# Performance work log

Measured on AMD Instinct MI355X. Metric: run time of the kernel, lower is better.

## Reference

```python
import jax, jax.numpy as jnp
import numpy as np

B, T, OBS, S, OUT, H = 128, 2048, 128, 128, 64, 64
SCALE = 0.05  # keep the linear recurrence numerically stable over T steps


def setup_inputs() -> dict:
    key = jax.random.key(0)
    ks = jax.random.split(key, 8)
    return {
        "obs": jax.random.normal(ks[0], (B, T, OBS), dtype=jnp.float32),
        "x0": jnp.zeros((B, S), dtype=jnp.float32),
        "A_T": SCALE * jax.random.normal(ks[1], (S, S), dtype=jnp.float32),
        "By_T": SCALE * jax.random.normal(ks[2], (OBS, S), dtype=jnp.float32),
        "Cu_T": SCALE * jax.random.normal(ks[3], (S, OUT), dtype=jnp.float32),
        "Duy_T": SCALE * jax.random.normal(ks[4], (OBS, OUT), dtype=jnp.float32),
        "log_stds": jnp.full((OUT,), -1.6094379124341003, dtype=jnp.float32),
        "W0": SCALE * jax.random.normal(ks[5], (H, OBS), dtype=jnp.float32),
        "b0": jnp.zeros((H,), dtype=jnp.float32),
        "W1": SCALE * jax.random.normal(ks[6], (H, H), dtype=jnp.float32),
        "b1": jnp.zeros((H,), dtype=jnp.float32),
        "W2": SCALE * jax.random.normal(ks[7], (1, H), dtype=jnp.float32),
        "b2": jnp.zeros((1,), dtype=jnp.float32),
        "dt": jnp.float32(0.01),
    }


def reference(obs, x0, A_T, By_T, Cu_T, Duy_T, log_stds, W0, b0, W1, b1, W2, b2, dt):
    def xdot(x, y):
        return x @ A_T + y @ By_T

    def step(x, y):
        # control output at current state, then RK4 integration of x' = A x + B y
        u = x @ Cu_T + y @ Duy_T                      # [B, OUT]
        k1 = xdot(x, y)
        k2 = xdot(x + dt * k1 / 2, y)
        k3 = xdot(x + dt * k2 / 2, y)
        k4 = xdot(x + dt * k3, y)
        x_next = x + dt / 6 * (k1 + 2 * k2 + 2 * k3 + k4)
        return x_next, u

    obs_t = jnp.swapaxes(obs, 0, 1)                   # [T, B, OBS]
    x_final, actions_t = jax.lax.scan(step, x0, obs_t)
    actions = jnp.swapaxes(actions_t, 0, 1)           # [B, T, OUT]

    logs = jnp.broadcast_to(log_stds, (actions.shape[0], actions.shape[1], log_stds.shape[0]))
    outputs = jnp.concatenate([actions, logs], axis=2)  # [B, T, 2*OUT]

    # value MLP: Linear -> tanh -> Linear -> tanh -> Linear
    h = jnp.tanh(obs @ W0.T + b0)
    h = jnp.tanh(h @ W1.T + b1)
    cur_value = (h @ W2.T + b2).reshape(-1)           # [B*T]

    return outputs, cur_value, x_final
```

## Files before the change

### kernel.cpp

```cpp
#include <hip/hip_runtime.h>
#include <hip/hip_bf16.h>

#define B_    128
#define T_    2048
#define OBS_  128
#define S_    128
#define OUT_  64
#define H_    64
#define NR    (B_*T_)
#define K_CH  32
#define C_CH  64
#define VOFF  (NR*2*OUT_)
#define XFOFF (VOFF + NR)

typedef __attribute__((ext_vector_type(8))) short short8v;
typedef __attribute__((ext_vector_type(4))) float f32x4;

__device__ __forceinline__ unsigned short f2bf_hw(float f){
  __hip_bfloat16 h = __float2bfloat16(f);
  union { __hip_bfloat16 hh; unsigned short u; } cv; cv.hh = h; return cv.u;
}
__device__ __forceinline__ unsigned int pk2(float a, float b){
  __hip_bfloat162 h = __float22bfloat162_rn(make_float2(a, b));
  union { __hip_bfloat162 h2; unsigned int u; } cv; cv.h2 = h; return cv.u;
}
__device__ __forceinline__ float bf2f(unsigned short h){
  return __uint_as_float(((unsigned int)h) << 16);
}
__device__ __forceinline__ float fast_tanh(float x){
  float z = __builtin_exp2f(x * 2.88539008f);
  return 1.f - 2.f * __builtin_amdgcn_rcpf(z + 1.f);
}

__global__ __launch_bounds__(256) void k_mm(const float* __restrict__ A,
                                            const float* __restrict__ B,
                                            float* __restrict__ C, int ldc){
  int e = blockIdx.x * 256 + threadIdx.x;
  int r = e >> 7, c = e & 127;
  float acc = 0.f;
  #pragma unroll 4
  for (int k = 0; k < 128; ++k) acc += A[r*128 + k] * B[k*128 + c];
  C[r*ldc + c] = acc;
}

__global__ __launch_bounds__(256) void k_mm2(const float* __restrict__ A_T,
                                             const float* __restrict__ A2,
                                             float* __restrict__ A3,
                                             float* __restrict__ A4){
  int e = blockIdx.x * 256 + threadIdx.x;
  int r = e >> 7, c = e & 127;
  float a3 = 0.f, a4 = 0.f;
  #pragma unroll 4
  for (int k = 0; k < 128; ++k){
    float l = A2[r*128 + k];
    a3 += l * A_T[k*128 + c];
    a4 += l * A2[k*128 + c];
  }
  A3[e] = a3; A4[e] = a4;
}

__global__ __launch_bounds__(256) void k_build(const float* __restrict__ A_T,
                                               const float* __restrict__ A2,
                                               const float* __restrict__ A3,
                                               const float* __restrict__ A4,
                                               const float* __restrict__ Cu_T,
                                               const float* __restrict__ Duy_T,
                                               const float* __restrict__ dtp,
                                               float* __restrict__ M,
                                               unsigned short* __restrict__ MmiT,
                                               float* __restrict__ P, float* __restrict__ Wcat,
                                               unsigned short* __restrict__ cubT){
  float dt = *dtp;
  float d2 = dt*dt*0.5f;
  float d3 = d2*dt*(1.f/3.f);
  float d4 = d3*dt*0.25f;
  int e = blockIdx.x * 256 + threadIdx.x;
  int r = e >> 7, c = e & 127;
  float eye = (r == c) ? 1.f : 0.f;
  float mi = dt*A_T[e] + d2*A2[e] + d3*A3[e] + d4*A4[e];
  M[e] = eye + mi;
  MmiT[c*128 + r] = f2bf_hw(mi);
  P[e] = dt*eye + d2*A_T[e] + d3*A2[e] + d4*A3[e];
  if (e < 128*64){
    int k = e >> 6, o = e & 63;
    Wcat[k*192 + 128 + o] = Duy_T[e];
    cubT[o*128 + k] = f2bf_hw(Cu_T[e]);
  }
}

__global__ __launch_bounds__(256) void k_gm2(const float* __restrict__ By_T,
                                             const float* __restrict__ Pp,
                                             const float* __restrict__ Mm,
                                             float* __restrict__ Wcat,
                                             float* __restrict__ sq1){
  int e = blockIdx.x * 256 + threadIdx.x;
  int r = e >> 7, c = e & 127;
  float ga = 0.f, m2 = 0.f;
  #pragma unroll 4
  for (int k = 0; k < 128; ++k){
    ga += By_T[r*128 + k] * Pp[k*128 + c];
    m2 += Mm[r*128 + k] * Mm[k*128 + c];
  }
  Wcat[r*192 + c] = ga;
  sq1[e] = m2;
}

__global__ __launch_bounds__(256) void k_m4cvt(const float* __restrict__ sq1,
                                               const float* __restrict__ Wcat,
                                               const float* __restrict__ W0,
                                               const float* __restrict__ W1,
                                               float* __restrict__ sq2,
                                               unsigned short* __restrict__ WbfT,
                                               unsigned short* __restrict__ W0bf,
                                               unsigned short* __restrict__ W1bf){
  int e = blockIdx.x * 256 + threadIdx.x;
  int r = e >> 7, c = e & 127;
  float m4 = 0.f;
  #pragma unroll 4
  for (int k = 0; k < 128; ++k) m4 += sq1[r*128 + k] * sq1[k*128 + c];
  sq2[e] = m4;
  for (int i = e; i < 24576; i += 16384)
    WbfT[(i % 192)*128 + (i / 192)] = f2bf_hw(Wcat[i]);
  if (e < 8192) W0bf[e] = f2bf_hw(W0[e]);
  if (e < 4096) W1bf[e] = f2bf_hw(W1[e]);
}

__global__ __launch_bounds__(256) void k_fused(const float* __restrict__ obs,
                                               const unsigned short* __restrict__ WbfT,
                                               const unsigned short* __restrict__ W0bf,
                                               const unsigned short* __restrict__ W1bf,
                                               const float* __restrict__ W2,
                                               const float* __restrict__ b0g,
                                               const float* __restrict__ b1g,
                                               const float* __restrict__ b2g,
                                               unsigned short* __restrict__ cuy,
                                               float* __restrict__ out){
  __shared__ __align__(16) unsigned short ylds[64*136];
  __shared__ __align__(16) unsigned short ct[2][16*200];
  __shared__ __align__(16) unsigned short h0l[64*80];
  __shared__ float pl[64][4];
  int tid = threadIdx.x;
  int lane = tid & 63, w = tid >> 6;
  size_t row0 = (size_t)blockIdx.x * 128;
  int colbase = w * 48;
  int colh    = w * 16;
  int lr = lane & 15;
  int lk = (lane >> 4) * 8;

  short8v bfrag[3][4];
  #pragma unroll
  for (int cf = 0; cf < 3; ++cf)
    #pragma unroll
    for (int kk = 0; kk < 4; ++kk)
      bfrag[cf][kk] = *(const short8v*)&WbfT[(size_t)(colbase + cf*16 + lr)*128 + kk*32 + lk];
  short8v bw0[4];
  #pragma unroll
  for (int kk = 0; kk < 4; ++kk)
    bw0[kk] = *(const short8v*)&W0bf[(size_t)(colh + lr)*128 + kk*32 + lk];
  short8v bw1[2];
  #pragma unroll
  for (int kk = 0; kk < 2; ++kk)
    bw1[kk] = *(const short8v*)&W1bf[(size_t)(colh + lr)*64 + kk*32 + lk];
  float b0v = b0g[colh + lr];
  float b1v = b1g[colh + lr];
  float w2v = W2[colh + lr];

  for (int h = 0; h < 2; ++h){
    {
      int base = tid * 32;
      int r = base >> 7, c0 = base & 127;
      const float* grow = obs + (row0 + h*64 + r) * 128;
      #pragma unroll
      for (int it = 0; it < 4; ++it){
        float4 a0 = *(const float4*)&grow[c0 + it*8];
        float4 a1 = *(const float4*)&grow[c0 + it*8 + 4];
        uint4 pv;
        pv.x = pk2(a0.x, a0.y); pv.y = pk2(a0.z, a0.w);
        pv.z = pk2(a1.x, a1.y); pv.w = pk2(a1.z, a1.w);
        *(uint4*)&ylds[r*136 + c0 + it*8] = pv;
      }
    }
    __syncthreads();
    for (int rfh = 0; rfh < 4; ++rfh){
      f32x4 acc0 = {0.f,0.f,0.f,0.f}, acc1 = {0.f,0.f,0.f,0.f}, acc2 = {0.f,0.f,0.f,0.f};
      f32x4 acch = {0.f,0.f,0.f,0.f};
      #pragma unroll
      for (int kk = 0; kk < 4; ++kk){
        short8v af = *(const short8v*)&ylds[(rfh*16 + lr)*136 + kk*32 + lk];
        acc0 = __builtin_amdgcn_mfma_f32_16x16x32_bf16(af, bfrag[0][kk], acc0, 0, 0, 0);
        acc1 = __builtin_amdgcn_mfma_f32_16x16x32_bf16(af, bfrag[1][kk], acc1, 0, 0, 0);
        acc2 = __builtin_amdgcn_mfma_f32_16x16x32_bf16(af, bfrag[2][kk], acc2, 0, 0, 0);
        acch = __builtin_amdgcn_mfma_f32_16x16x32_bf16(af, bw0[kk],     acch, 0, 0, 0);
      }
      int hrow = rfh*16 + (lane >> 4)*4;
      int crow = (lane >> 4)*4;
      unsigned short* ctb = ct[rfh & 1];
      #pragma unroll
      for (int j = 0; j < 4; ++j){
        ctb[(crow + j)*200 + colbase      + lr] = f2bf_hw(acc0[j]);
        ctb[(crow + j)*200 + colbase + 16 + lr] = f2bf_hw(acc1[j]);
        ctb[(crow + j)*200 + colbase + 32 + lr] = f2bf_hw(acc2[j]);
        h0l[(hrow + j)*80 + colh + lr]          = f2bf_hw(fast_tanh(acch[j] + b0v));
      }
      __syncthreads();
      for (int li = tid; li < 16*24; li += 256){
        int r = li / 24, seg = li % 24;
        *(uint4*)&cuy[(row0 + h*64 + rfh*16 + r)*192 + seg*8] = *(const uint4*)&ctb[r*200 + seg*8];
      }
    }
    for (int rf = 0; rf < 4; ++rf){
      f32x4 acc = {b1v, b1v, b1v, b1v};
      #pragma unroll
      for (int kk = 0; kk < 2; ++kk){
        short8v af = *(const short8v*)&h0l[(rf*16 + lr)*80 + kk*32 + lk];
        acc = __builtin_amdgcn_mfma_f32_16x16x32_bf16(af, bw1[kk], acc, 0, 0, 0);
      }
      float4 vpart;
      #pragma unroll
      for (int j = 0; j < 4; ++j) (&vpart.x)[j] = fast_tanh(acc[j]) * w2v;
      #pragma unroll
      for (int m = 1; m < 16; m <<= 1){
        vpart.x += __shfl_xor(vpart.x, m);
        vpart.y += __shfl_xor(vpart.y, m);
        vpart.z += __shfl_xor(vpart.z, m);
        vpart.w += __shfl_xor(vpart.w, m);
      }
      if (lr == 0){
        int hrow = rf*16 + (lane >> 4)*4;
        #pragma unroll
        for (int j = 0; j < 4; ++j) pl[hrow + j][w] = (&vpart.x)[j];
      }
    }
    __syncthreads();
    if (tid < 64)
      out[(size_t)VOFF + row0 + h*64 + tid] = pl[tid][0] + pl[tid][1] + pl[tid][2] + pl[tid][3] + b2g[0];
    __syncthreads();
  }
}

__global__ __launch_bounds__(256) void k_phase1(const unsigned short* __restrict__ cuy,
                                                const unsigned short* __restrict__ MmiT,
                                                float* __restrict__ Dd){
  __shared__ __align__(16) unsigned short xwA[16*136];
  __shared__ __align__(16) unsigned short xwB[16*136];
  int tid = threadIdx.x;
  int lane = tid & 63, w = tid >> 6;
  int lr = lane & 15, lg = lane >> 4;
  int pr = blockIdx.x >> 3, bi = blockIdx.x & 7;
  int b0 = bi*16;
  int ciA = 2*pr, ciB = 2*pr + 1;
  int t0A = ciA*K_CH, t0B = ciB*K_CH;
  int colbase = w*32;

  short8v bm[2][4];
  #pragma unroll
  for (int ctt = 0; ctt < 2; ++ctt)
    #pragma unroll
    for (int kk = 0; kk < 4; ++kk)
      bm[ctt][kk] = *(const short8v*)&MmiT[(size_t)(colbase + ctt*16 + lr)*128 + kk*32 + lg*8];

  f32x4 accA[2], accB[2];
  #pragma unroll
  for (int ctt = 0; ctt < 2; ++ctt)
    #pragma unroll
    for (int j = 0; j < 4; ++j){
      size_t rb = (size_t)(b0 + lg*4 + j)*T_;
      accA[ctt][j] = bf2f(cuy[(rb + t0A)*192 + colbase + ctt*16 + lr]);
      accB[ctt][j] = bf2f(cuy[(rb + t0B)*192 + colbase + ctt*16 + lr]);
    }

  for (int s = 1; s < K_CH; ++s){
    unsigned short cnA[2][4], cnB[2][4];
    #pragma unroll
    for (int ctt = 0; ctt < 2; ++ctt)
      #pragma unroll
      for (int j = 0; j < 4; ++j){
        size_t rb = (size_t)(b0 + lg*4 + j)*T_;
        cnA[ctt][j] = cuy[(rb + t0A + s)*192 + colbase + ctt*16 + lr];
        cnB[ctt][j] = cuy[(rb + t0B + s)*192 + colbase + ctt*16 + lr];
      }
    #pragma unroll
    for (int ctt = 0; ctt < 2; ++ctt)
      #pragma unroll
      for (int j = 0; j < 4; ++j){
        xwA[(lg*4 + j)*136 + colbase + ctt*16 + lr] = f2bf_hw(accA[ctt][j]);
        xwB[(lg*4 + j)*136 + colbase + ctt*16 + lr] = f2bf_hw(accB[ctt][j]);
      }
    __syncthreads();
    short8v afA[4], afB[4];
    #pragma unroll
    for (int kk = 0; kk < 4; ++kk){
      afA[kk] = *(const short8v*)&xwA[lr*136 + kk*32 + lg*8];
      afB[kk] = *(const short8v*)&xwB[lr*136 + kk*32 + lg*8];
    }
    __syncthreads();
    #pragma unroll
    for (int ctt = 0; ctt < 2; ++ctt)
      #pragma unroll
      for (int kk = 0; kk < 4; ++kk)
        accA[ctt] = __builtin_amdgcn_mfma_f32_16x16x32_bf16(afA[kk], bm[ctt][kk], accA[ctt], 0, 0, 0);
    #pragma unroll
    for (int ctt = 0; ctt < 2; ++ctt)
      #pragma unroll
      for (int kk = 0; kk < 4; ++kk)
        accB[ctt] = __builtin_amdgcn_mfma_f32_16x16x32_bf16(afB[kk], bm[ctt][kk], accB[ctt], 0, 0, 0);
    #pragma unroll
    for (int ctt = 0; ctt < 2; ++ctt)
      #pragma unroll
      for (int j = 0; j < 4; ++j){
        accA[ctt][j] += bf2f(cnA[ctt][j]);
        accB[ctt][j] += bf2f(cnB[ctt][j]);
      }
  }
  #pragma unroll
  for (int ctt = 0; ctt < 2; ++ctt)
    #pragma unroll
    for (int j = 0; j < 4; ++j){
      Dd[(size_t)ciA*16384 + (size_t)(b0 + lg*4 + j)*128 + colbase + ctt*16 + lr] = accA[ctt][j];
      Dd[(size_t)ciB*16384 + (size_t)(b0 + lg*4 + j)*128 + colbase + ctt*16 + lr] = accB[ctt][j];
    }
}

__global__ __launch_bounds__(256) void k_combine(const float* __restrict__ Mk,
                                                 const float* __restrict__ Dd,
                                                 const float* __restrict__ x0,
                                                 float* __restrict__ XS,
                                                 float* __restrict__ xfin){
  __shared__ float xl[128];
  __shared__ float pl[256];
  int tid = threadIdx.x;
  int b = blockIdx.x;
  int c = tid & 127, h = tid >> 7;
  float mreg[64];
  #pragma unroll
  for (int j = 0; j < 64; ++j) mreg[j] = Mk[(64*h + j)*128 + c];
  if (tid < 128) xl[tid] = x0[(size_t)b*128 + tid];
  float dcur = (tid < 128) ? Dd[(size_t)b*128 + tid] : 0.f;
  __syncthreads();
  for (int i = 0; i < C_CH; ++i){
    if (tid < 128) XS[(size_t)i*16384 + (size_t)b*128 + tid] = xl[tid];
    float dnext = 0.f;
    if (i + 1 < C_CH && tid < 128)
      dnext = Dd[(size_t)(i+1)*16384 + (size_t)b*128 + tid];
    float part = 0.f;
    #pragma unroll
    for (int jj = 0; jj < 64; jj += 4){
      float4 xv = *(const float4*)&xl[64*h + jj];
      part += xv.x*mreg[jj] + xv.y*mreg[jj+1] + xv.z*mreg[jj+2] + xv.w*mreg[jj+3];
    }
    pl[tid] = part;
    __syncthreads();
    if (tid < 128)
      xl[tid] = pl[tid] + pl[tid + 128] + dcur;
    __syncthreads();
    dcur = dnext;
  }
  if (tid < 128) xfin[(size_t)b*128 + tid] = xl[tid];
}

__global__ __launch_bounds__(256) void k_phase3(const unsigned short* __restrict__ cuy,
                                                const unsigned short* __restrict__ MmiT,
                                                const unsigned short* __restrict__ cubT,
                                                const float* __restrict__ XS,
                                                const float* __restrict__ ls,
                                                float* __restrict__ out){
  __shared__ __align__(16) unsigned short xwA[16*136];
  __shared__ __align__(16) unsigned short xwB[16*136];
  int tid = threadIdx.x;
  int lane = tid & 63, w = tid >> 6;
  int lr = lane & 15, lg = lane >> 4;
  int pr = blockIdx.x >> 3, bi = blockIdx.x & 7;
  int b0 = bi*16;
  int ciA = 2*pr, ciB = 2*pr + 1;
  int t0A = ciA*K_CH, t0B = ciB*K_CH;
  int colbase = w*32;
  int ucolbase = w*16;
  float lsv = ls[ucolbase + lr];

  short8v bm[2][4];
  #pragma unroll
  for (int ctt = 0; ctt < 2; ++ctt)
    #pragma unroll
    for (int kk = 0; kk < 4; ++kk)
      bm[ctt][kk] = *(const short8v*)&MmiT[(size_t)(colbase + ctt*16 + lr)*128 + kk*32 + lg*8];
  short8v bc[4];
  #pragma unroll
  for (int kk = 0; kk < 4; ++kk)
    bc[kk] = *(const short8v*)&cubT[(size_t)(ucolbase + lr)*128 + kk*32 + lg*8];

  f32x4 accA[2], accB[2];
  #pragma unroll
  for (int ctt = 0; ctt < 2; ++ctt)
    #pragma unroll
    for (int j = 0; j < 4; ++j){
      size_t xb = (size_t)(b0 + lg*4 + j)*128 + colbase + ctt*16 + lr;
      accA[ctt][j] = XS[(size_t)ciA*16384 + xb];
      accB[ctt][j] = XS[(size_t)ciB*16384 + xb];
    }

  for (int s = 0; s < K_CH; ++s){
    f32x4 auA, auB;
    #pragma unroll
    for (int j = 0; j < 4; ++j){
      size_t rb = (size_t)(b0 + lg*4 + j)*T_;
      auA[j] = bf2f(cuy[(rb + t0A + s)*192 + 128 + ucolbase + lr]);
      auB[j] = bf2f(cuy[(rb + t0B + s)*192 + 128 + ucolbase + lr]);
    }
    unsigned short cnA[2][4], cnB[2][4];
    if (s + 1 < K_CH){
      #pragma unroll
      for (int ctt = 0; ctt < 2; ++ctt)
        #pragma unroll
        for (int j = 0; j < 4; ++j){
          size_t rb = (size_t)(b0 + lg*4 + j)*T_;
          cnA[ctt][j] = cuy[(rb + t0A + s)*192 + colbase + ctt*16 + lr];
          cnB[ctt][j] = cuy[(rb + t0B + s)*192 + colbase + ctt*16 + lr];
        }
    }
    #pragma unroll
    for (int ctt = 0; ctt < 2; ++ctt)
      #pragma unroll
      for (int j = 0; j < 4; ++j){
        xwA[(lg*4 + j)*136 + colbase + ctt*16 + lr] = f2bf_hw(accA[ctt][j]);
        xwB[(lg*4 + j)*136 + colbase + ctt*16 + lr] = f2bf_hw(accB[ctt][j]);
      }
    __syncthreads();
    short8v afA[4], afB[4];
    #pragma unroll
    for (int kk = 0; kk < 4; ++kk){
      afA[kk] = *(const short8v*)&xwA[lr*136 + kk*32 + lg*8];
      afB[kk] = *(const short8v*)&xwB[lr*136 + kk*32 + lg*8];
    }
    __syncthreads();
    #pragma unroll
    for (int kk = 0; kk < 4; ++kk){
      auA = __builtin_amdgcn_mfma_f32_16x16x32_bf16(afA[kk], bc[kk], auA, 0, 0, 0);
      auB = __builtin_amdgcn_mfma_f32_16x16x32_bf16(afB[kk], bc[kk], auB, 0, 0, 0);
    }
    #pragma unroll
    for (int j = 0; j < 4; ++j){
      size_t rb = (size_t)(b0 + lg*4 + j)*T_;
      out[(rb + t0A + s)*128 + ucolbase + lr]       = auA[j];
      out[(rb + t0A + s)*128 + 64 + ucolbase + lr]  = lsv;
      out[(rb + t0B + s)*128 + ucolbase + lr]       = auB[j];
      out[(rb + t0B + s)*128 + 64 + ucolbase + lr]  = lsv;
    }
    if (s + 1 < K_CH){
      #pragma unroll
      for (int ctt = 0; ctt < 2; ++ctt)
        #pragma unroll
        for (int kk = 0; kk < 4; ++kk)
          accA[ctt] = __builtin_amdgcn_mfma_f32_16x16x32_bf16(afA[kk], bm[ctt][kk], accA[ctt], 0, 0, 0);
      #pragma unroll
      for (int ctt = 0; ctt < 2; ++ctt)
        #pragma unroll
        for (int kk = 0; kk < 4; ++kk)
          accB[ctt] = __builtin_amdgcn_mfma_f32_16x16x32_bf16(afB[kk], bm[ctt][kk], accB[ctt], 0, 0, 0);
      #pragma unroll
      for (int ctt = 0; ctt < 2; ++ctt)
        #pragma unroll
        for (int j = 0; j < 4; ++j){
          accA[ctt][j] += bf2f(cnA[ctt][j]);
          accB[ctt][j] += bf2f(cnB[ctt][j]);
        }
    }
  }
}

extern "C" void kernel_launch(void* const* d_in, const int* in_sizes, int n_in,
                              void* d_out, int out_size, void* d_ws, size_t ws_size,
                              hipStream_t stream){
  const float* obs  = (const float*)d_in[0];
  const float* x0   = (const float*)d_in[1];
  const float* A_T  = (const float*)d_in[2];
  const float* By_T = (const float*)d_in[3];
  const float* Cu_T = (const float*)d_in[4];
  const float* Duy_T= (const float*)d_in[5];
  const float* ls   = (const float*)d_in[6];
  const float* W0   = (const float*)d_in[7];
  const float* b0   = (const float*)d_in[8];
  const float* W1   = (const float*)d_in[9];
  const float* b1   = (const float*)d_in[10];
  const float* W2   = (const float*)d_in[11];
  const float* b2   = (const float*)d_in[12];
  const float* dt   = (const float*)d_in[13];
  float* out = (float*)d_out;

  char* ws = (char*)d_ws;
  unsigned short* cuy = (unsigned short*)(ws + 0);
  float* A2     = (float*)(ws + 100663296);
  float* A3     = (float*)(ws + 100728832);
  float* A4     = (float*)(ws + 100794368);
  float* Mm     = (float*)(ws + 100859904);
  float* Pp     = (float*)(ws + 100925440);
  float* Mk     = (float*)(ws + 100990976);
  float* sq1    = (float*)(ws + 101056512);
  float* sq2    = (float*)(ws + 101122048);
  unsigned short* MmiT = (unsigned short*)(ws + 101187584);
  float* Wcat   = (float*)(ws + 101255168);
  unsigned short* cubT = (unsigned short*)(ws + 101353472);
  float* Dd     = (float*)(ws + 101387264);
  float* XS     = (float*)(ws + 105581568);
  unsigned short* WbfT = (unsigned short*)Pp;
  unsigned short* W0bf = (unsigned short*)A3;
  unsigned short* W1bf = (unsigned short*)A4;

  k_mm   <<<64, 256, 0, stream>>>(A_T, A_T, A2, 128);
  k_mm2  <<<64, 256, 0, stream>>>(A_T, A2, A3, A4);
  k_build<<<64, 256, 0, stream>>>(A_T, A2, A3, A4, Cu_T, Duy_T, dt, Mm, MmiT, Pp, Wcat, cubT);
  k_gm2  <<<64, 256, 0, stream>>>(By_T, Pp, Mm, Wcat, sq1);
  k_m4cvt<<<64, 256, 0, stream>>>(sq1, Wcat, W0, W1, sq2, WbfT, W0bf, W1bf);
  k_mm   <<<64, 256, 0, stream>>>(sq2, sq2, sq1, 128);
  k_mm   <<<64, 256, 0, stream>>>(sq1, sq1, sq2, 128);
  k_mm   <<<64, 256, 0, stream>>>(sq2, sq2, Mk, 128);

  k_fused<<<NR/128, 256, 0, stream>>>(obs, WbfT, W0bf, W1bf, W2, b0, b1, b2, cuy, out);
  k_phase1<<<(C_CH/2)*8, 256, 0, stream>>>(cuy, MmiT, Dd);
  k_combine<<<B_, 256, 0, stream>>>(Mk, Dd, x0, XS, out + XFOFF);
  k_phase3<<<(C_CH/2)*8, 256, 0, stream>>>(cuy, MmiT, cubT, XS, ls, out);
}
```

Before: 277.1 us.

## Rewrite phase1 chunk scan as single-wave transposed MFMA with bpermute exchange

The chunk-local recurrence kernel now runs one 64-lane wave per (chunk, batch-tile) block instead of a 4-wave block that handled two chunks. The matrix product is transposed so the full state row lives in one wave's accumulators, and the bf16 operand is rebuilt with ds_bpermute lane shuffles. This removes the per-step LDS round trip and the two __syncthreads on the 31-step serial chain. It also switches to vectorized ushort4 loads and float4 stores. In exchange each wave holds 32 matrix fragments in registers (high VGPR use) and issues 8 MFMAs per k-slice serially.

Measured after the change: 289.0 us. 4.3% more time.

```diff
diff --git a/kernel.cpp b/kernel.cpp
--- a/kernel.cpp
+++ b/kernel.cpp
@@ -238,87 +238,76 @@
   }
 }
 
-__global__ __launch_bounds__(256) void k_phase1(const unsigned short* __restrict__ cuy,
-                                                const unsigned short* __restrict__ MmiT,
-                                                float* __restrict__ Dd){
-  __shared__ __align__(16) unsigned short xwA[16*136];
-  __shared__ __align__(16) unsigned short xwB[16*136];
-  int tid = threadIdx.x;
-  int lane = tid & 63, w = tid >> 6;
+__global__ __launch_bounds__(64) void k_phase1(const unsigned short* __restrict__ cuy,
+                                               const unsigned short* __restrict__ MmiT,
+                                               float* __restrict__ Dd){
+  int lane = threadIdx.x;
   int lr = lane & 15, lg = lane >> 4;
-  int pr = blockIdx.x >> 3, bi = blockIdx.x & 7;
-  int b0 = bi*16;
-  int ciA = 2*pr, ciB = 2*pr + 1;
-  int t0A = ciA*K_CH, t0B = ciB*K_CH;
-  int colbase = w*32;
-
-  short8v bm[2][4];
-  #pragma unroll
-  for (int ctt = 0; ctt < 2; ++ctt)
+  int ci = blockIdx.x >> 3, b0 = (blockIdx.x & 7) * 16;
+  int t0 = ci * K_CH;
+  int addrA = ((((lg & 1)*2)    )*16 + lr) * 4;
+  int addrB = ((((lg & 1)*2) + 1)*16 + lr) * 4;
+  bool hiSel = (lg >> 1) != 0;
+
+  short8v am[8][4];
+  #pragma unroll
+  for (int fo = 0; fo < 8; ++fo)
     #pragma unroll
     for (int kk = 0; kk < 4; ++kk)
-      bm[ctt][kk] = *(const short8v*)&MmiT[(size_t)(colbase + ctt*16 + lr)*128 + kk*32 + lg*8];
-
-  f32x4 accA[2], accB[2];
-  #pragma unroll
-  for (int ctt = 0; ctt < 2; ++ctt)
-    #pragma unroll
-    for (int j = 0; j < 4; ++j){
-      size_t rb = (size_t)(b0 + lg*4 + j)*T_;
-      accA[ctt][j] = bf2f(cuy[(rb + t0A)*192 + colbase + ctt*16 + lr]);
-      accB[ctt][j] = bf2f(cuy[(rb + t0B)*192 + colbase + ctt*16 + lr]);
-    }
+      am[fo][kk] = *(const short8v*)&MmiT[(size_t)(fo*16 + lr)*128 + kk*32 + lg*8];
+
+  size_t rowb = ((size_t)(b0 + lr) * T_ + t0) * 192;
+  f32x4 acc[8];
+  #pragma unroll
+  for (int fo = 0; fo < 8; ++fo){
+    ushort4 c4 = *(const ushort4*)&cuy[rowb + fo*16 + lg*4];
+    acc[fo][0] = bf2f(c4.x); acc[fo][1] = bf2f(c4.y);
+    acc[fo][2] = bf2f(c4.z); acc[fo][3] = bf2f(c4.w);
+  }
 
   for (int s = 1; s < K_CH; ++s){
-    unsigned short cnA[2][4], cnB[2][4];
-    #pragma unroll
-    for (int ctt = 0; ctt < 2; ++ctt)
-      #pragma unroll
-      for (int j = 0; j < 4; ++j){
-        size_t rb = (size_t)(b0 + lg*4 + j)*T_;
-        cnA[ctt][j] = cuy[(rb + t0A + s)*192 + colbase + ctt*16 + lr];
-        cnB[ctt][j] = cuy[(rb + t0B + s)*192 + colbase + ctt*16 + lr];
-      }
-    #pragma unroll
-    for (int ctt = 0; ctt < 2; ++ctt)
-      #pragma unroll
-      for (int j = 0; j < 4; ++j){
-        xwA[(lg*4 + j)*136 + colbase + ctt*16 + lr] = f2bf_hw(accA[ctt][j]);
-        xwB[(lg*4 + j)*136 + colbase + ctt*16 + lr] = f2bf_hw(accB[ctt][j]);
-      }
-    __syncthreads();
-    short8v afA[4], afB[4];
+    ushort4 cn[8];
+    #pragma unroll
+    for (int fo = 0; fo < 8; ++fo)
+      cn[fo] = *(const ushort4*)&cuy[rowb + (size_t)s*192 + fo*16 + lg*4];
+    unsigned int pk[8][2];
+    #pragma unroll
+    for (int fo = 0; fo < 8; ++fo){
+      pk[fo][0] = pk2(acc[fo][0], acc[fo][1]);
+      pk[fo][1] = pk2(acc[fo][2], acc[fo][3]);
+    }
+    short8v Bf[4];
     #pragma unroll
     for (int kk = 0; kk < 4; ++kk){
-      afA[kk] = *(const short8v*)&xwA[lr*136 + kk*32 + lg*8];
-      afB[kk] = *(const short8v*)&xwB[lr*136 + kk*32 + lg*8];
-    }
-    __syncthreads();
-    #pragma unroll
-    for (int ctt = 0; ctt < 2; ++ctt)
+      unsigned int w0a = (unsigned int)__builtin_amdgcn_ds_bpermute(addrA, (int)pk[2*kk  ][0]);
+      unsigned int w0b = (unsigned int)__builtin_amdgcn_ds_bpermute(addrA, (int)pk[2*kk+1][0]);
+      unsigned int w1a = (unsigned int)__builtin_amdgcn_ds_bpermute(addrA, (int)pk[2*kk  ][1]);
+      unsigned int w1b = (unsigned int)__builtin_amdgcn_ds_bpermute(addrA, (int)pk[2*kk+1][1]);
+      unsigned int w2a = (unsigned int)__builtin_amdgcn_ds_bpermute(addrB, (int)pk[2*kk  ][0]);
+      unsigned int w2b = (unsigned int)__builtin_amdgcn_ds_bpermute(addrB, (int)pk[2*kk+1][0]);
+      unsigned int w3a = (unsigned int)__builtin_amdgcn_ds_bpermute(addrB, (int)pk[2*kk  ][1]);
+      unsigned int w3b = (unsigned int)__builtin_amdgcn_ds_bpermute(addrB, (int)pk[2*kk+1][1]);
+      union { unsigned int u[4]; short8v v; } bu;
+      bu.u[0] = hiSel ? w0b : w0a;
+      bu.u[1] = hiSel ? w1b : w1a;
+      bu.u[2] = hiSel ? w2b : w2a;
+      bu.u[3] = hiSel ? w3b : w3a;
+      Bf[kk] = bu.v;
+    }
+    #pragma unroll
+    for (int fo = 0; fo < 8; ++fo){
       #pragma unroll
       for (int kk = 0; kk < 4; ++kk)
-        accA[ctt] = __builtin_amdgcn_mfma_f32_16x16x32_bf16(afA[kk], bm[ctt][kk], accA[ctt], 0, 0, 0);
-    #pragma unroll
-    for (int ctt = 0; ctt < 2; ++ctt)
-      #pragma unroll
-      for (int kk = 0; kk < 4; ++kk)
-        accB[ctt] = __builtin_amdgcn_mfma_f32_16x16x32_bf16(afB[kk], bm[ctt][kk], accB[ctt], 0, 0, 0);
-    #pragma unroll
-    for (int ctt = 0; ctt < 2; ++ctt)
-      #pragma unroll
-      for (int j = 0; j < 4; ++j){
-        accA[ctt][j] += bf2f(cnA[ctt][j]);
-        accB[ctt][j] += bf2f(cnB[ctt][j]);
-      }
-  }
-  #pragma unroll
-  for (int ctt = 0; ctt < 2; ++ctt)
-    #pragma unroll
-    for (int j = 0; j < 4; ++j){
-      Dd[(size_t)ciA*16384 + (size_t)(b0 + lg*4 + j)*128 + colbase + ctt*16 + lr] = accA[ctt][j];
-      Dd[(size_t)ciB*16384 + (size_t)(b0 + lg*4 + j)*128 + colbase + ctt*16 + lr] = accB[ctt][j];
-    }
+        acc[fo] = __builtin_amdgcn_mfma_f32_16x16x32_bf16(am[fo][kk], Bf[kk], acc[fo], 0, 0, 0);
+      acc[fo][0] += bf2f(cn[fo].x); acc[fo][1] += bf2f(cn[fo].y);
+      acc[fo][2] += bf2f(cn[fo].z); acc[fo][3] += bf2f(cn[fo].w);
+    }
+  }
+  #pragma unroll
+  for (int fo = 0; fo < 8; ++fo){
+    float4 st; st.x = acc[fo][0]; st.y = acc[fo][1]; st.z = acc[fo][2]; st.w = acc[fo][3];
+    *(float4*)&Dd[(size_t)ci*16384 + (size_t)(b0 + lr)*128 + fo*16 + lg*4] = st;
+  }
 }
 
 __global__ __launch_bounds__(256) void k_combine(const float* __restrict__ Mk,
@@ -515,7 +504,7 @@
   k_mm   <<<64, 256, 0, stream>>>(sq2, sq2, Mk, 128);
 
   k_fused<<<NR/128, 256, 0, stream>>>(obs, WbfT, W0bf, W1bf, W2, b0, b1, b2, cuy, out);
-  k_phase1<<<(C_CH/2)*8, 256, 0, stream>>>(cuy, MmiT, Dd);
+  k_phase1<<<C_CH*8, 64, 0, stream>>>(cuy, MmiT, Dd);
   k_combine<<<B_, 256, 0, stream>>>(Mk, Dd, x0, XS, out + XFOFF);
   k_phase3<<<(C_CH/2)*8, 256, 0, stream>>>(cuy, MmiT, cubT, XS, ls, out);
 }
```
